# Performance work log

Hardware: AMD Instinct MI355X
Metric: run time of the kernel (lower is better)

Reference implementation:

```python
import jax, jax.numpy as jnp
import numpy as np


def setup_inputs() -> dict:
    key = jax.random.key(0)
    k1, k2, k3, k4 = jax.random.split(key, 4)
    B, N, M, D = 8, 2048, 2048, 256
    x = jax.random.normal(k1, (B, N, D), dtype=jnp.float32)
    Fi = jax.random.normal(k2, (B, M, D), dtype=jnp.float32)
    # nn.Linear(dim, dim) params (W applied as x @ W.T + b); scale like torch default
    bound = 1.0 / np.sqrt(D)
    W = jax.random.uniform(k3, (D, D), dtype=jnp.float32, minval=-bound, maxval=bound)
    b = jax.random.uniform(k4, (D,), dtype=jnp.float32, minval=-bound, maxval=bound)
    return {"x": x, "Fi": Fi, "W": W, "b": b}


def reference(x, Fi, W, b):
    # x: [B, N, D], Fi: [B, M, D]
    q = jnp.einsum("bnd,ed->bne", x, W) + b          # linear projection
    scores = jnp.einsum("bnd,bmd->bnm", q, Fi)        # QK^T (no scaling in original)
    attn = jax.nn.softmax(scores, axis=-1)            # softmax over keys
    out = jnp.einsum("bnm,bmd->bnd", attn, Fi)        # attention @ V (V = Fi)
    return out
```

## Files before the change

kernel.cpp:

```cpp
#include <hip/hip_runtime.h>
#include <hip/hip_bf16.h>

typedef _Float16 half8 __attribute__((ext_vector_type(8)));
typedef float floatx4 __attribute__((ext_vector_type(4)));

#define MFMA16H(a, b, c) __builtin_amdgcn_mfma_f32_16x16x32_f16((a), (b), (c), 0, 0, 0)

static constexpr int Bb = 8, Nn = 2048, Mm = 2048, Dd = 256;

__device__ inline void async16(const void* g, void* l)
{
    __builtin_amdgcn_global_load_lds((const __attribute__((address_space(1))) unsigned int*)g,
                                     (__attribute__((address_space(3))) unsigned int*)l,
                                     16, 0, 0);
}

__device__ inline half8 cvt8h(const float* __restrict__ p)
{
    float4 f0 = *reinterpret_cast<const float4*>(p);
    float4 f1 = *reinterpret_cast<const float4*>(p + 4);
    half8 r;
    r[0] = (_Float16)f0.x; r[1] = (_Float16)f0.y; r[2] = (_Float16)f0.z; r[3] = (_Float16)f0.w;
    r[4] = (_Float16)f1.x; r[5] = (_Float16)f1.y; r[6] = (_Float16)f1.z; r[7] = (_Float16)f1.w;
    return r;
}

__device__ inline void cvt8h_split(const float* __restrict__ p, half8& h, half8& l)
{
    float4 f0 = *reinterpret_cast<const float4*>(p);
    float4 f1 = *reinterpret_cast<const float4*>(p + 4);
    float f[8] = {f0.x, f0.y, f0.z, f0.w, f1.x, f1.y, f1.z, f1.w};
#pragma unroll
    for (int i = 0; i < 8; ++i) {
        _Float16 hh = (_Float16)f[i];
        h[i] = hh;
        l[i] = (_Float16)(f[i] - (float)hh);
    }
}

__global__ __launch_bounds__(256, 4)
void prep_kernel(const float* __restrict__ Fi, const float* __restrict__ W,
                 _Float16* __restrict__ FiH, _Float16* __restrict__ FiT,
                 _Float16* __restrict__ Wh, _Float16* __restrict__ Wl)
{
    const int bid = blockIdx.x;
    const int t = threadIdx.x;

    if (bid >= 1024) {
        const size_t base = (size_t)(bid - 1024) * 2048 + t * 8;
        half8 h, l;
        cvt8h_split(W + base, h, l);
        *(half8*)(Wh + base) = h;
        *(half8*)(Wl + base) = l;
        return;
    }

    __shared__ __align__(16) unsigned short tile[64][72];
    const int b  = bid >> 7;
    const int mt = (bid >> 2) & 31;
    const int dt = bid & 3;
    {
        const int i = t >> 2, jc = (t & 3) * 16;
        const float* src = Fi + ((size_t)b * Mm + mt * 64 + i) * Dd + dt * 64 + jc;
        union { half8 v; uint4 u; } p0, p1;
        p0.v = cvt8h(src);
        p1.v = cvt8h(src + 8);
        *(uint4*)&tile[i][jc]     = p0.u;
        *(uint4*)&tile[i][jc + 8] = p1.u;
        unsigned short* dh = reinterpret_cast<unsigned short*>(FiH)
            + ((size_t)b * Mm + mt * 64 + i) * Dd + dt * 64 + jc;
        *(uint4*)dh       = p0.u;
        *(uint4*)(dh + 8) = p1.u;
    }
    __syncthreads();
    {
        const int d = t >> 2, mc = (t & 3) * 16;
        unsigned short* dst = reinterpret_cast<unsigned short*>(FiT)
            + ((size_t)b * Dd + dt * 64 + d) * Mm + mt * 64 + mc;
        union { uint4 v[2]; unsigned short s[16]; } u;
#pragma unroll
        for (int s = 0; s < 16; ++s) u.s[s] = tile[mc + s][d];
        *(uint4*)dst       = u.v[0];
        *(uint4*)(dst + 8) = u.v[1];
    }
}

__global__ __launch_bounds__(256, 2)
void qproj_kernel(const float* __restrict__ x, const _Float16* __restrict__ Wh,
                  const _Float16* __restrict__ Wl, const float* __restrict__ bias,
                  _Float16* __restrict__ q)
{
    __shared__ __align__(16) _Float16 sWh[256 * 32];
    __shared__ __align__(16) _Float16 sWl[256 * 32];

    const int tid = threadIdx.x;
    const int lane = tid & 63, w = tid >> 6;
    const int lo = lane & 15, hi = lane >> 4;
    const long r0 = (long)blockIdx.x * 32;

    floatx4 acc[2][4];
#pragma unroll
    for (int rt = 0; rt < 2; ++rt)
#pragma unroll
        for (int j = 0; j < 4; ++j) acc[rt][j] = (floatx4)0.0f;

    const int se = lane >> 2, sc = lane & 3;

    for (int k0 = 0; k0 < 256; k0 += 32) {
        __syncthreads();
#pragma unroll
        for (int j = 0; j < 4; ++j) {
            const int e0 = (w * 4 + j) * 16;
            const int e = e0 + se;
            const int gc = sc ^ (e & 3);
            async16(Wh + (size_t)e * Dd + k0 + gc * 8, sWh + e0 * 32);
            async16(Wl + (size_t)e * Dd + k0 + gc * 8, sWl + e0 * 32);
        }
        __syncthreads();

        half8 ah[2], al[2];
#pragma unroll
        for (int rt = 0; rt < 2; ++rt)
            cvt8h_split(x + (size_t)(r0 + rt * 16 + lo) * Dd + k0 + hi * 8, ah[rt], al[rt]);
#pragma unroll
        for (int jj = 0; jj < 4; ++jj) {
            const int e = (w * 4 + jj) * 16 + lo;
            half8 bh = *reinterpret_cast<const half8*>(&sWh[(e & 255) * 32 + ((hi ^ (e & 3)) * 8)]);
            half8 bl = *reinterpret_cast<const half8*>(&sWl[(e & 255) * 32 + ((hi ^ (e & 3)) * 8)]);
#pragma unroll
            for (int rt = 0; rt < 2; ++rt) {
                acc[rt][jj] = MFMA16H(ah[rt], bh, acc[rt][jj]);
                acc[rt][jj] = MFMA16H(ah[rt], bl, acc[rt][jj]);
                acc[rt][jj] = MFMA16H(al[rt], bh, acc[rt][jj]);
            }
        }
    }
#pragma unroll
    for (int jj = 0; jj < 4; ++jj) {
        const int e = (w * 4 + jj) * 16 + lo;
        const float bv = bias[e];
#pragma unroll
        for (int rt = 0; rt < 2; ++rt)
#pragma unroll
            for (int r = 0; r < 4; ++r)
                q[(size_t)(r0 + rt * 16 + hi * 4 + r) * Dd + e] = (_Float16)(acc[rt][jj][r] + bv);
    }
}

__global__ __launch_bounds__(256, 2)
void flash_kernel(const _Float16* __restrict__ q, const _Float16* __restrict__ FiH,
                  const _Float16* __restrict__ FiT, _Float16* __restrict__ o_part,
                  float* __restrict__ m_part, float* __restrict__ l_part)
{
    __shared__ __align__(16) _Float16 sFiA[32 * 256];
    __shared__ __align__(16) _Float16 sFiB[32 * 256];
    __shared__ __align__(16) _Float16 sFiTA[256 * 32];
    __shared__ __align__(16) _Float16 sFiTB[256 * 32];
    __shared__ __align__(16) _Float16 sP[4][32 * 40];

    const int bid = blockIdx.x;
    const int b  = bid & 7;
    const int u  = bid >> 3;
    const int nt = u & 15;
    const int kh = u >> 4;
    const int tid = threadIdx.x;
    const int lane = tid & 63, w = tid >> 6;
    const int lo = lane & 15, hi = lane >> 4;
    const int nbase = nt * 128 + w * 32;

    const _Float16* fH = FiH + (size_t)b * Mm * Dd;
    const _Float16* fT = FiT + (size_t)b * Dd * Mm;

    half8 qf[2][8];
    const _Float16* qb = q + ((size_t)b * Nn + nbase + lo) * Dd + hi * 8;
#pragma unroll
    for (int rt = 0; rt < 2; ++rt)
#pragma unroll
        for (int kk = 0; kk < 8; ++kk)
            qf[rt][kk] = *reinterpret_cast<const half8*>(qb + rt * 16 * Dd + kk * 32);

    half8 ones;
#pragma unroll
    for (int i = 0; i < 8; ++i) ones[i] = (_Float16)1.0f;

    floatx4 o[2][16];
    floatx4 ol[2];
#pragma unroll
    for (int rt = 0; rt < 2; ++rt) {
#pragma unroll
        for (int t = 0; t < 16; ++t) o[rt][t] = (floatx4)0.0f;
        ol[rt] = (floatx4)0.0f;
    }
    float m_i[2][4];
#pragma unroll
    for (int rt = 0; rt < 2; ++rt)
#pragma unroll
        for (int r = 0; r < 4; ++r) m_i[rt][r] = -INFINITY;

    auto stage = [&](int it, _Float16* dFi, _Float16* dFiT) {
        const int key0 = kh * 512 + it * 32;
#pragma unroll
        for (int j = 0; j < 4; ++j) {
            const int rbase = (w * 4 + j) * 2;
            const int r = rbase + (lane >> 5);
            const int kp = 2 * (r & 15) + (r >> 4);
            const int gc = (lane & 31) ^ (r & 7);
            async16(fH + (size_t)(key0 + kp) * Dd + gc * 8, dFi + rbase * 256);
        }
#pragma unroll
        for (int j = 0; j < 4; ++j) {
            const int rbase = (w + j * 4) * 16;
            const int r = rbase + (lane >> 2);
            const int gc = (lane & 3) ^ (r & 3);
            async16(fT + (size_t)r * Mm + key0 + gc * 8, dFiT + rbase * 32);
        }
    };

    auto compute = [&](const _Float16* SFI, const _Float16* SFIT) {
        floatx4 s[2][2];
#pragma unroll
        for (int rt = 0; rt < 2; ++rt)
#pragma unroll
            for (int st = 0; st < 2; ++st) s[rt][st] = (floatx4)0.0f;
#pragma unroll
        for (int st = 0; st < 2; ++st) {
            const int row = st * 16 + lo;
#pragma unroll
            for (int kk = 0; kk < 8; ++kk) {
                half8 bv = *reinterpret_cast<const half8*>(
                    SFI + row * 256 + (((kk * 4 + hi) ^ (lo & 7)) * 8));
                s[0][st] = MFMA16H(qf[0][kk], bv, s[0][st]);
                s[1][st] = MFMA16H(qf[1][kk], bv, s[1][st]);
            }
        }

        float mn[2][4];
        bool chg = false;
#pragma unroll
        for (int rt = 0; rt < 2; ++rt)
#pragma unroll
            for (int r = 0; r < 4; ++r) {
                float mc = fmaxf(s[rt][0][r], s[rt][1][r]);
                mc = fmaxf(mc, __shfl_xor(mc, 1));
                mc = fmaxf(mc, __shfl_xor(mc, 2));
                mc = fmaxf(mc, __shfl_xor(mc, 4));
                mc = fmaxf(mc, __shfl_xor(mc, 8));
                mn[rt][r] = fmaxf(m_i[rt][r], mc);
                chg = chg || (mn[rt][r] > m_i[rt][r]);
            }
        if (__any(chg)) {
#pragma unroll
            for (int rt = 0; rt < 2; ++rt) {
                float al4[4];
#pragma unroll
                for (int r = 0; r < 4; ++r) {
                    al4[r] = __expf(m_i[rt][r] - mn[rt][r]);
                    m_i[rt][r] = mn[rt][r];
                }
#pragma unroll
                for (int t = 0; t < 16; ++t) {
                    floatx4 ot = o[rt][t];
#pragma unroll
                    for (int r = 0; r < 4; ++r) ot[r] *= al4[r];
                    o[rt][t] = ot;
                }
#pragma unroll
                for (int r = 0; r < 4; ++r) ol[rt][r] *= al4[r];
            }
        }
#pragma unroll
        for (int rt = 0; rt < 2; ++rt)
#pragma unroll
            for (int r = 0; r < 4; ++r) {
                union { _Float16 h[2]; unsigned u; } pk;
                pk.h[0] = (_Float16)__expf(s[rt][0][r] - m_i[rt][r]);
                pk.h[1] = (_Float16)__expf(s[rt][1][r] - m_i[rt][r]);
                *reinterpret_cast<unsigned*>(
                    &sP[w][(rt * 16 + hi * 4 + r) * 40 + 2 * lo]) = pk.u;
            }

        half8 pa0 = *reinterpret_cast<const half8*>(&sP[w][lo * 40 + hi * 8]);
        half8 pa1 = *reinterpret_cast<const half8*>(&sP[w][(16 + lo) * 40 + hi * 8]);
#pragma unroll
        for (int t = 0; t < 16; ++t) {
            half8 bv = *reinterpret_cast<const half8*>(
                SFIT + (t * 16 + lo) * 32 + ((hi ^ (lo & 3)) * 8));
            o[0][t] = MFMA16H(pa0, bv, o[0][t]);
            o[1][t] = MFMA16H(pa1, bv, o[1][t]);
        }
        ol[0] = MFMA16H(pa0, ones, ol[0]);
        ol[1] = MFMA16H(pa1, ones, ol[1]);
    };

    stage(0, sFiA, sFiTA);
    for (int it = 0; it < 16; it += 2) {
        __syncthreads();
        stage(it + 1, sFiB, sFiTB);
        compute(sFiA, sFiTA);
        __syncthreads();
        if (it + 2 < 16) stage(it + 2, sFiA, sFiTA);
        compute(sFiB, sFiTB);
    }

#pragma unroll
    for (int rt = 0; rt < 2; ++rt)
#pragma unroll
        for (int r = 0; r < 4; ++r) {
            const long gq = (long)b * Nn + nbase + rt * 16 + hi * 4 + r;
            const size_t obase = ((size_t)kh * (Bb * Nn) + gq) * Dd;
#pragma unroll
            for (int t = 0; t < 16; ++t)
                o_part[obase + t * 16 + lo] = (_Float16)o[rt][t][r];
            if (lo == 0) {
                m_part[(size_t)kh * (Bb * Nn) + gq] = m_i[rt][r];
                l_part[(size_t)kh * (Bb * Nn) + gq] = ol[rt][r];
            }
        }
}

__global__ __launch_bounds__(256, 8)
void merge_kernel(const _Float16* __restrict__ o_part, const float* __restrict__ m_part,
                  const float* __restrict__ l_part, float* __restrict__ out)
{
    const int row = blockIdx.x;
    const int col = threadIdx.x;
    float m[4], l[4];
#pragma unroll
    for (int k = 0; k < 4; ++k) {
        m[k] = m_part[(size_t)k * (Bb * Nn) + row];
        l[k] = l_part[(size_t)k * (Bb * Nn) + row];
    }
    float M = fmaxf(fmaxf(m[0], m[1]), fmaxf(m[2], m[3]));
    float denom = 0.f, acc = 0.f;
#pragma unroll
    for (int k = 0; k < 4; ++k) {
        const float wk = __expf(m[k] - M);
        denom += wk * l[k];
        acc += wk * (float)o_part[((size_t)k * (Bb * Nn) + row) * Dd + col];
    }
    out[(size_t)row * Dd + col] = acc / denom;
}

extern "C" void kernel_launch(void* const* d_in, const int* in_sizes, int n_in,
                              void* d_out, int out_size, void* d_ws, size_t ws_size,
                              hipStream_t stream)
{
    const float* x    = (const float*)d_in[0];
    const float* Fi   = (const float*)d_in[1];
    const float* W    = (const float*)d_in[2];
    const float* bias = (const float*)d_in[3];
    float* out = (float*)d_out;

    _Float16* q_ws = (_Float16*)d_ws;
    _Float16* FiH  = q_ws + (size_t)Bb * Nn * Dd;
    _Float16* FiT  = FiH + (size_t)Bb * Mm * Dd;
    _Float16* Wh   = FiT + (size_t)Bb * Dd * Mm;
    _Float16* Wl   = Wh + (size_t)Dd * Dd;
    _Float16* o_part = Wl + (size_t)Dd * Dd;
    float* m_part  = (float*)(o_part + (size_t)4 * Bb * Nn * Dd);
    float* l_part  = m_part + (size_t)4 * Bb * Nn;

    hipLaunchKernelGGL(prep_kernel, dim3(1056), dim3(256), 0, stream, Fi, W, FiH, FiT, Wh, Wl);
    hipLaunchKernelGGL(qproj_kernel, dim3(512), dim3(256), 0, stream, x, Wh, Wl, bias, q_ws);
    hipLaunchKernelGGL(flash_kernel, dim3(512), dim3(256), 0, stream, q_ws, FiH, FiT,
                       o_part, m_part, l_part);
    hipLaunchKernelGGL(merge_kernel, dim3(16384), dim3(256), 0, stream, o_part, m_part, l_part, out);
}
```

Measured before the change: 216.7 us.

## Double-buffer qproj W tiles, swizzle prep transpose, reshape P staging, batch merge rows

The q projection now double-buffers the W hi/lo tiles in shared memory, so the async load of the next k-slice overlaps the MFMAs on the current one. The prep transpose tile drops its padding in favour of an XOR swizzle, and the flash kernel no longer interleaves keys when staging Fi. Its P scratch is restructured to write separate halves with a 36-element row stride. The merge kernel processes 8 rows per block, cutting the grid from 16384 blocks to 2048. Together these aim to cut LDS bank conflicts, exposed load latency and launch overhead, at the cost of double the qproj shared memory and a possible change in P/key pairing correctness.

```diff
diff --git a/kernel.cpp b/kernel.cpp
--- a/kernel.cpp
+++ b/kernel.cpp
@@ -55,18 +55,19 @@
         return;
     }
 
-    __shared__ __align__(16) unsigned short tile[64][72];
+    __shared__ __align__(16) unsigned short tile[64][64];
     const int b  = bid >> 7;
     const int mt = (bid >> 2) & 31;
     const int dt = bid & 3;
     {
         const int i = t >> 2, jc = (t & 3) * 16;
+        const int pc = ((jc >> 4) ^ (i >> 4)) * 16;
         const float* src = Fi + ((size_t)b * Mm + mt * 64 + i) * Dd + dt * 64 + jc;
         union { half8 v; uint4 u; } p0, p1;
         p0.v = cvt8h(src);
         p1.v = cvt8h(src + 8);
-        *(uint4*)&tile[i][jc]     = p0.u;
-        *(uint4*)&tile[i][jc + 8] = p1.u;
+        *(uint4*)&tile[i][pc]     = p0.u;
+        *(uint4*)&tile[i][pc + 8] = p1.u;
         unsigned short* dh = reinterpret_cast<unsigned short*>(FiH)
             + ((size_t)b * Mm + mt * 64 + i) * Dd + dt * 64 + jc;
         *(uint4*)dh       = p0.u;
@@ -79,7 +80,10 @@
             + ((size_t)b * Dd + dt * 64 + d) * Mm + mt * 64 + mc;
         union { uint4 v[2]; unsigned short s[16]; } u;
 #pragma unroll
-        for (int s = 0; s < 16; ++s) u.s[s] = tile[mc + s][d];
+        for (int s = 0; s < 16; ++s) {
+            const int row = mc + s;
+            u.s[s] = tile[row][((d >> 4) ^ (row >> 4)) * 16 + (d & 15)];
+        }
         *(uint4*)dst       = u.v[0];
         *(uint4*)(dst + 8) = u.v[1];
     }
@@ -90,8 +94,10 @@
                   const _Float16* __restrict__ Wl, const float* __restrict__ bias,
                   _Float16* __restrict__ q)
 {
-    __shared__ __align__(16) _Float16 sWh[256 * 32];
-    __shared__ __align__(16) _Float16 sWl[256 * 32];
+    __shared__ __align__(16) _Float16 sWhA[256 * 32];
+    __shared__ __align__(16) _Float16 sWlA[256 * 32];
+    __shared__ __align__(16) _Float16 sWhB[256 * 32];
+    __shared__ __align__(16) _Float16 sWlB[256 * 32];
 
     const int tid = threadIdx.x;
     const int lane = tid & 63, w = tid >> 6;
@@ -106,18 +112,18 @@
 
     const int se = lane >> 2, sc = lane & 3;
 
-    for (int k0 = 0; k0 < 256; k0 += 32) {
-        __syncthreads();
+    auto stage = [&](int k0, _Float16* dWh, _Float16* dWl) {
 #pragma unroll
         for (int j = 0; j < 4; ++j) {
             const int e0 = (w * 4 + j) * 16;
             const int e = e0 + se;
             const int gc = sc ^ (e & 3);
-            async16(Wh + (size_t)e * Dd + k0 + gc * 8, sWh + e0 * 32);
-            async16(Wl + (size_t)e * Dd + k0 + gc * 8, sWl + e0 * 32);
-        }
-        __syncthreads();
-
+            async16(Wh + (size_t)e * Dd + k0 + gc * 8, dWh + e0 * 32);
+            async16(Wl + (size_t)e * Dd + k0 + gc * 8, dWl + e0 * 32);
+        }
+    };
+
+    auto compute = [&](int k0, const _Float16* SWh, const _Float16* SWl) {
         half8 ah[2], al[2];
 #pragma unroll
         for (int rt = 0; rt < 2; ++rt)
@@ -125,8 +131,8 @@
 #pragma unroll
         for (int jj = 0; jj < 4; ++jj) {
             const int e = (w * 4 + jj) * 16 + lo;
-            half8 bh = *reinterpret_cast<const half8*>(&sWh[(e & 255) * 32 + ((hi ^ (e & 3)) * 8)]);
-            half8 bl = *reinterpret_cast<const half8*>(&sWl[(e & 255) * 32 + ((hi ^ (e & 3)) * 8)]);
+            half8 bh = *reinterpret_cast<const half8*>(&SWh[(e & 255) * 32 + ((hi ^ (e & 3)) * 8)]);
+            half8 bl = *reinterpret_cast<const half8*>(&SWl[(e & 255) * 32 + ((hi ^ (e & 3)) * 8)]);
 #pragma unroll
             for (int rt = 0; rt < 2; ++rt) {
                 acc[rt][jj] = MFMA16H(ah[rt], bh, acc[rt][jj]);
@@ -134,6 +140,16 @@
                 acc[rt][jj] = MFMA16H(al[rt], bh, acc[rt][jj]);
             }
         }
+    };
+
+    stage(0, sWhA, sWlA);
+    for (int k0 = 0; k0 < 256; k0 += 64) {
+        __syncthreads();
+        stage(k0 + 32, sWhB, sWlB);
+        compute(k0, sWhA, sWlA);
+        __syncthreads();
+        if (k0 + 64 < 256) stage(k0 + 64, sWhA, sWlA);
+        compute(k0 + 32, sWhB, sWlB);
     }
 #pragma unroll
     for (int jj = 0; jj < 4; ++jj) {
@@ -156,7 +172,7 @@
     __shared__ __align__(16) _Float16 sFiB[32 * 256];
     __shared__ __align__(16) _Float16 sFiTA[256 * 32];
     __shared__ __align__(16) _Float16 sFiTB[256 * 32];
-    __shared__ __align__(16) _Float16 sP[4][32 * 40];
+    __shared__ __align__(16) _Float16 sP[4][32 * 36];
 
     const int bid = blockIdx.x;
     const int b  = bid & 7;
@@ -203,9 +219,8 @@
         for (int j = 0; j < 4; ++j) {
             const int rbase = (w * 4 + j) * 2;
             const int r = rbase + (lane >> 5);
-            const int kp = 2 * (r & 15) + (r >> 4);
             const int gc = (lane & 31) ^ (r & 7);
-            async16(fH + (size_t)(key0 + kp) * Dd + gc * 8, dFi + rbase * 256);
+            async16(fH + (size_t)(key0 + r) * Dd + gc * 8, dFi + rbase * 256);
         }
 #pragma unroll
         for (int j = 0; j < 4; ++j) {
@@ -272,15 +287,14 @@
         for (int rt = 0; rt < 2; ++rt)
 #pragma unroll
             for (int r = 0; r < 4; ++r) {
-                union { _Float16 h[2]; unsigned u; } pk;
-                pk.h[0] = (_Float16)__expf(s[rt][0][r] - m_i[rt][r]);
-                pk.h[1] = (_Float16)__expf(s[rt][1][r] - m_i[rt][r]);
-                *reinterpret_cast<unsigned*>(
-                    &sP[w][(rt * 16 + hi * 4 + r) * 40 + 2 * lo]) = pk.u;
-            }
-
-        half8 pa0 = *reinterpret_cast<const half8*>(&sP[w][lo * 40 + hi * 8]);
-        half8 pa1 = *reinterpret_cast<const half8*>(&sP[w][(16 + lo) * 40 + hi * 8]);
+                _Float16 p0 = (_Float16)__expf(s[rt][0][r] - m_i[rt][r]);
+                _Float16 p1 = (_Float16)__expf(s[rt][1][r] - m_i[rt][r]);
+                sP[w][(rt * 16 + hi * 4 + r) * 36 + lo]      = p0;
+                sP[w][(rt * 16 + hi * 4 + r) * 36 + 16 + lo] = p1;
+            }
+
+        half8 pa0 = *reinterpret_cast<const half8*>(&sP[w][lo * 36 + hi * 8]);
+        half8 pa1 = *reinterpret_cast<const half8*>(&sP[w][(16 + lo) * 36 + hi * 8]);
 #pragma unroll
         for (int t = 0; t < 16; ++t) {
             half8 bv = *reinterpret_cast<const half8*>(
@@ -322,23 +336,26 @@
 void merge_kernel(const _Float16* __restrict__ o_part, const float* __restrict__ m_part,
                   const float* __restrict__ l_part, float* __restrict__ out)
 {
-    const int row = blockIdx.x;
     const int col = threadIdx.x;
-    float m[4], l[4];
-#pragma unroll
-    for (int k = 0; k < 4; ++k) {
-        m[k] = m_part[(size_t)k * (Bb * Nn) + row];
-        l[k] = l_part[(size_t)k * (Bb * Nn) + row];
-    }
-    float M = fmaxf(fmaxf(m[0], m[1]), fmaxf(m[2], m[3]));
-    float denom = 0.f, acc = 0.f;
-#pragma unroll
-    for (int k = 0; k < 4; ++k) {
-        const float wk = __expf(m[k] - M);
-        denom += wk * l[k];
-        acc += wk * (float)o_part[((size_t)k * (Bb * Nn) + row) * Dd + col];
-    }
-    out[(size_t)row * Dd + col] = acc / denom;
+#pragma unroll
+    for (int rr = 0; rr < 8; ++rr) {
+        const int row = blockIdx.x * 8 + rr;
+        float m[4], l[4];
+#pragma unroll
+        for (int k = 0; k < 4; ++k) {
+            m[k] = m_part[(size_t)k * (Bb * Nn) + row];
+            l[k] = l_part[(size_t)k * (Bb * Nn) + row];
+        }
+        float M = fmaxf(fmaxf(m[0], m[1]), fmaxf(m[2], m[3]));
+        float denom = 0.f, acc = 0.f;
+#pragma unroll
+        for (int k = 0; k < 4; ++k) {
+            const float wk = __expf(m[k] - M);
+            denom += wk * l[k];
+            acc += wk * (float)o_part[((size_t)k * (Bb * Nn) + row) * Dd + col];
+        }
+        out[(size_t)row * Dd + col] = acc / denom;
+    }
 }
 
 extern "C" void kernel_launch(void* const* d_in, const int* in_sizes, int n_in,
@@ -364,5 +381,5 @@
     hipLaunchKernelGGL(qproj_kernel, dim3(512), dim3(256), 0, stream, x, Wh, Wl, bias, q_ws);
     hipLaunchKernelGGL(flash_kernel, dim3(512), dim3(256), 0, stream, q_ws, FiH, FiT,
                        o_part, m_part, l_part);
-    hipLaunchKernelGGL(merge_kernel, dim3(16384), dim3(256), 0, stream, o_part, m_part, l_part, out);
-}
+    hipLaunchKernelGGL(merge_kernel, dim3(2048), dim3(256), 0, stream, o_part, m_part, l_part, out);
+}
```

Result: faster. 212.0 us (-2.2%).
